# Kernel optimization log

Measured on AMD Instinct MI355X. Metric: run time of the kernel, lower is better.

The kernel has to match this reference:

```python
import jax, jax.numpy as jnp
import numpy as np

D_MODEL = 1024
N_HEAD = 16
D_K = D_MODEL // N_HEAD


def setup_inputs() -> dict:
    key = jax.random.key(0)
    ks = jax.random.split(key, 11)
    B, T = 2, 2048
    s = 1.0 / np.sqrt(D_MODEL)
    return {
        "q": jax.random.normal(ks[0], (B, T, D_MODEL), jnp.float32),
        "k": jax.random.normal(ks[1], (B, T, D_MODEL), jnp.float32),
        "v": jax.random.normal(ks[2], (B, T, D_MODEL), jnp.float32),
        "w_q": jax.random.normal(ks[3], (D_MODEL, D_MODEL), jnp.float32) * s,
        "b_q": jax.random.normal(ks[4], (D_MODEL,), jnp.float32) * 0.01,
        "w_k": jax.random.normal(ks[5], (D_MODEL, D_MODEL), jnp.float32) * s,
        "b_k": jax.random.normal(ks[6], (D_MODEL,), jnp.float32) * 0.01,
        "w_v": jax.random.normal(ks[7], (D_MODEL, D_MODEL), jnp.float32) * s,
        "b_v": jax.random.normal(ks[8], (D_MODEL,), jnp.float32) * 0.01,
        "w_o": jax.random.normal(ks[9], (D_MODEL, D_MODEL), jnp.float32) * s,
        "b_o": jax.random.normal(ks[10], (D_MODEL,), jnp.float32) * 0.01,
    }


def reference(q, k, v, w_q, b_q, w_k, b_k, w_v, b_v, w_o, b_o):
    B, T, _ = q.shape
    # QKV projections -> [B, H, T, d_k]
    def proj(x, w, b):
        return (jnp.einsum('btd,de->bte', x, w) + b).reshape(B, T, N_HEAD, D_K).transpose(0, 2, 1, 3)
    qh = proj(q, w_q, b_q)
    kh = proj(k, w_k, b_k)
    vh = proj(v, w_v, b_v)
    scale = jnp.float32(1.0 / np.sqrt(D_K))
    scores = jnp.einsum('bhqd,bhkd->bhqk', qh, kh) * scale  # [B,H,T,T]
    attn = jax.nn.softmax(scores, axis=-1)
    # dropout is identity in eval mode
    out = jnp.einsum('bhqk,bhkd->bhqd', attn, vh)  # [B,H,T,d_k]
    out = out.transpose(0, 2, 1, 3).reshape(B, T, N_HEAD * D_K)
    return jnp.einsum('btd,de->bte', out, w_o) + b_o
```

## Files before the change

### kernel.cpp

```cpp
#include <hip/hip_runtime.h>
#include <stdint.h>

#define DEVI static __device__ __forceinline__

typedef float f32x4 __attribute__((ext_vector_type(4)));
typedef float f32x16 __attribute__((ext_vector_type(16)));
typedef short s16x8 __attribute__((ext_vector_type(8)));
typedef unsigned short u16x4 __attribute__((ext_vector_type(4)));
typedef uint32_t u32x2 __attribute__((ext_vector_type(2)));
typedef uint32_t u32x4 __attribute__((ext_vector_type(4)));

DEVI unsigned short f2bf(float f) {
  union { float f; uint32_t u; } v; v.f = f;
  uint32_t u = v.u;
  return (unsigned short)((u + 0x7fffu + ((u >> 16) & 1u)) >> 16);
}

DEVI float bf2f(unsigned short u) {
  union { uint32_t u; float f; } v;
  v.u = ((uint32_t)u) << 16;
  return v.f;
}

DEVI uint32_t cvtpk(float lo, float hi) {
  uint32_t r;
  asm("v_cvt_pk_bf16_f32 %0, %1, %2" : "=v"(r) : "v"(lo), "v"(hi));
  return r;
}

DEVI float fexp2(float x) {
#if __has_builtin(__builtin_amdgcn_exp2f)
  return __builtin_amdgcn_exp2f(x);
#else
  return exp2f(x);
#endif
}

DEVI float max3(float a, float b, float c) {
  float r;
  asm("v_max3_f32 %0, %1, %2, %3" : "=v"(r) : "v"(a), "v"(b), "v"(c));
  return r;
}

DEVI void pl32swap(uint32_t& a, uint32_t& b) {
#if __has_builtin(__builtin_amdgcn_permlane32_swap)
  u32x2 r = __builtin_amdgcn_permlane32_swap(a, b, false, false);
  a = r[0]; b = r[1];
#else
  asm("v_permlane32_swap_b32 %0, %1" : "+v"(a), "+v"(b));
#endif
}

DEVI float swap_half(float x, int hi) {
  uint32_t a = __float_as_uint(x), b = a;
  pl32swap(a, b);
  return hi ? __uint_as_float(a) : __uint_as_float(b);
}

DEVI void g2l16(const void* g, void* l) {
  __builtin_amdgcn_global_load_lds(
      (const __attribute__((address_space(1))) void*)g,
      (__attribute__((address_space(3))) void*)l, 16, 0, 0);
}

DEVI float vmax16(const f32x16& v) {
  float a = max3(v[0], v[1], v[2]);
  float b = max3(v[3], v[4], v[5]);
  float c = max3(v[6], v[7], v[8]);
  float d = max3(v[9], v[10], v[11]);
  float e = max3(v[12], v[13], v[14]);
  float x = max3(a, b, c);
  float y = max3(d, e, v[15]);
  return fmaxf(x, y);
}

__global__ __launch_bounds__(256) void k_prep(
    const float* __restrict__ q, const float* __restrict__ k,
    const float* __restrict__ v, unsigned short* __restrict__ qkv,
    const float* __restrict__ w0, const float* __restrict__ w1,
    const float* __restrict__ w2, const float* __restrict__ w3,
    unsigned short* __restrict__ t0, unsigned short* __restrict__ t1,
    unsigned short* __restrict__ t2, unsigned short* __restrict__ t3) {
  __shared__ float tile[32][33];
  const int bx = blockIdx.x;
  if (bx < 3072) {
    const int y = bx >> 10;
    const float* in = y == 0 ? q : y == 1 ? k : v;
    unsigned short* o = qkv + (size_t)y * 4194304;
    int idx = (bx & 1023) * 256 + threadIdx.x;
    for (int i = idx * 4; i < 4194304; i += 1048576) {
      f32x4 x = *(const f32x4*)(in + i);
      u16x4 r;
      for (int j = 0; j < 4; ++j) r[j] = f2bf(x[j]);
      *(u16x4*)(o + i) = r;
    }
  } else {
    const int wb = bx - 3072;
    const int z = wb >> 10, tb = wb & 1023;
    const float* w = z == 0 ? w0 : z == 1 ? w1 : z == 2 ? w2 : w3;
    unsigned short* wt = z == 0 ? t0 : z == 1 ? t1 : z == 2 ? t2 : t3;
    const int n0 = (tb & 31) * 32, k0 = (tb >> 5) * 32;
    const int tx = threadIdx.x & 31, ty = threadIdx.x >> 5;
    for (int j = 0; j < 4; ++j)
      tile[ty + j * 8][tx] = w[(size_t)(k0 + ty + j * 8) * 1024 + n0 + tx];
    __syncthreads();
    for (int j = 0; j < 4; ++j)
      wt[(size_t)(n0 + ty + j * 8) * 1024 + k0 + tx] = f2bf(tile[tx][ty + j * 8]);
  }
}

__global__ __launch_bounds__(256) void k_gemm_multi(
    const unsigned short* A0, const unsigned short* A1, const unsigned short* A2,
    const unsigned short* B0, const unsigned short* B1, const unsigned short* B2,
    const float* c0, const float* c1, const float* c2,
    void* o0, void* o1, void* o2, int mode0) {
  constexpr int K = 1024;
  const int z = blockIdx.y;
  const unsigned short* A = z == 0 ? A0 : z == 1 ? A1 : A2;
  const unsigned short* Bt = z == 0 ? B0 : z == 1 ? B1 : B2;
  const float* bias = z == 0 ? c0 : z == 1 ? c1 : c2;
  void* outp = z == 0 ? o0 : z == 1 ? o1 : o2;
  const int MODE = mode0 + z;

  __shared__ __align__(16) unsigned short As[128 * 64];
  __shared__ __align__(16) unsigned short Bs[64 * 64];
  const int tid = threadIdx.x;
  const int lane = tid & 63, w = tid >> 6;
  const int g = lane >> 4, c = lane & 15;
  const int wgid = (blockIdx.x & 7) * 64 + (blockIdx.x >> 3);
  const int bm = wgid >> 4, bn = wgid & 15;
  const int m0 = bm * 128, n0 = bn * 64;
  const int wr = w >> 1, wc = w & 1;
  f32x4 acc[4][2] = {};

  for (int kt = 0; kt < 16; ++kt) {
    const int k0 = kt * 64;
    __syncthreads();
#pragma unroll
    for (int it = 0; it < 4; ++it) {
      int e = it * 256 + tid;
      int row = e >> 3, cwp = (e & 7) ^ (row & 7);
      g2l16(A + (size_t)(m0 + row) * K + k0 + cwp * 8,
            (char*)As + (it * 256 + (w << 6)) * 16);
    }
#pragma unroll
    for (int it = 0; it < 2; ++it) {
      int e = it * 256 + tid;
      int row = e >> 3, cwp = (e & 7) ^ (row & 7);
      g2l16(Bt + (size_t)(n0 + row) * K + k0 + cwp * 8,
            (char*)Bs + (it * 256 + (w << 6)) * 16);
    }
    __syncthreads();
    for (int kk = 0; kk < 2; ++kk) {
      s16x8 af[4], bfr[2];
      for (int mi = 0; mi < 4; ++mi) {
        int row = wr * 64 + mi * 16 + c;
        int ch = (kk * 4 + g) ^ (row & 7);
        af[mi] = *(const s16x8*)((const char*)As + row * 128 + ch * 16);
      }
      for (int ni = 0; ni < 2; ++ni) {
        int row = wc * 32 + ni * 16 + c;
        int ch = (kk * 4 + g) ^ (row & 7);
        bfr[ni] = *(const s16x8*)((const char*)Bs + row * 128 + ch * 16);
      }
      for (int mi = 0; mi < 4; ++mi)
        for (int ni = 0; ni < 2; ++ni)
          acc[mi][ni] = __builtin_amdgcn_mfma_f32_16x16x32_bf16(
              af[mi], bfr[ni], acc[mi][ni], 0, 0, 0);
    }
  }

  if (MODE == 0 || MODE == 1) {
    unsigned short* out = (unsigned short*)outp;
    const float scale = (MODE == 0) ? 0.1803368801111204f : 1.0f;
    for (int mi = 0; mi < 4; ++mi)
      for (int ni = 0; ni < 2; ++ni) {
        int row = m0 + wr * 64 + mi * 16 + g * 4;
        int col = n0 + wc * 32 + ni * 16 + c;
        float bb = bias[col];
        for (int r = 0; r < 4; ++r)
          out[(size_t)(row + r) * 1024 + col] = f2bf((acc[mi][ni][r] + bb) * scale);
      }
  } else if (MODE == 2) {
    unsigned short* vt = (unsigned short*)outp;
    const int bq = m0 >> 11, t0 = m0 & 2047;
    for (int mi = 0; mi < 4; ++mi)
      for (int ni = 0; ni < 2; ++ni) {
        int rowb = wr * 64 + mi * 16 + g * 4;
        int coll = wc * 32 + ni * 16 + c;
        float bb = bias[n0 + coll];
        u16x4 pk;
        for (int r = 0; r < 4; ++r) pk[r] = f2bf(acc[mi][ni][r] + bb);
        *(u16x4*)(vt + (size_t)(bq * 1024 + n0 + coll) * 2048 + t0 + rowb) = pk;
      }
  } else {
    float* out = (float*)outp;
    for (int mi = 0; mi < 4; ++mi)
      for (int ni = 0; ni < 2; ++ni) {
        int row = m0 + wr * 64 + mi * 16 + g * 4;
        int col = n0 + wc * 32 + ni * 16 + c;
        float bb = bias[col];
        for (int r = 0; r < 4; ++r)
          out[(size_t)(row + r) * 1024 + col] = acc[mi][ni][r] + bb;
      }
  }
}

__global__ __launch_bounds__(256) void k_attn(const unsigned short* __restrict__ Qp,
                                              const unsigned short* __restrict__ Kp,
                                              const unsigned short* __restrict__ Vt,
                                              unsigned short* __restrict__ Po0,
                                              unsigned short* __restrict__ Po1,
                                              float2* __restrict__ ml) {
  __shared__ __align__(16) unsigned short Ks[2][4096];
  __shared__ __align__(16) unsigned short Vs[2][4096];
  const int tid = threadIdx.x;
  const int lane = tid & 63, w = tid >> 6;
  const int l31 = lane & 31, hi = lane >> 5;
  const int blk = (blockIdx.x & 7) * 128 + (blockIdx.x >> 3);
  const int half = blk & 1, qt = (blk >> 1) & 15, bh = blk >> 5;
  const int b = bh >> 4, h = bh & 15;
  const int m0 = qt * 128 + w * 32;
  const size_t qkBase = (size_t)b * 2048 * 1024 + (size_t)h * 64;
  const size_t vtBase = ((size_t)b * 1024 + h * 64) * 2048;

  const unsigned short* qrow = Qp + qkBase + (size_t)(m0 + l31) * 1024;
  s16x8 bq[4];
#pragma unroll
  for (int s = 0; s < 4; ++s)
    bq[s] = *(const s16x8*)(qrow + s * 16 + hi * 8);

  const int r0 = tid >> 3, c0 = tid & 7;
  const int csw = (c0 ^ (r0 & 7)) * 8;
  const unsigned short* ks0 = Kp + qkBase + (size_t)half * 1048576 +
                              (size_t)r0 * 1024 + csw;
  const unsigned short* vs0 = Vt + vtBase + (size_t)r0 * 2048 + half * 1024 + csw;
  const int ldw = w * 1024;

  auto stage = [&](int buf, int t) {
    const size_t ko = (size_t)t * 65536;
    const int vo = t * 64;
    char* kb = (char*)&Ks[buf][0];
    char* vb = (char*)&Vs[buf][0];
    g2l16(ks0 + ko, kb + ldw);
    g2l16(ks0 + ko + 32 * 1024, kb + 4096 + ldw);
    g2l16(vs0 + vo, vb + ldw);
    g2l16(vs0 + vo + 32 * 2048, vb + 4096 + ldw);
  };

  float m_run = -1e30f;
  f32x16 o0 = {}, o1 = {}, la = {};
  const u32x4 onev = {0x3F803F80u, 0x3F803F80u, 0x3F803F80u, 0x3F803F80u};
  const s16x8 ones = *(const s16x8*)&onev;

  stage(0, 0);
  __syncthreads();

  const int rch = l31 & 7;

#pragma unroll 1
  for (int t = 0; t < 16; ++t) {
    const int cur = t & 1;
    if (t < 15) stage(cur ^ 1, t + 1);
    const char* ks = (const char*)&Ks[cur][0];
    const char* vs = (const char*)&Vs[cur][0];

    f32x16 s0 = {}, s1 = {};
    __builtin_amdgcn_s_setprio(1);
#pragma unroll
    for (int ds = 0; ds < 4; ++ds) {
      int ch = (2 * ds + hi) ^ rch;
      s16x8 a0 = *(const s16x8*)(ks + l31 * 128 + ch * 16);
      s16x8 a1 = *(const s16x8*)(ks + (32 + l31) * 128 + ch * 16);
      s0 = __builtin_amdgcn_mfma_f32_32x32x16_bf16(a0, bq[ds], s0, 0, 0, 0);
      s1 = __builtin_amdgcn_mfma_f32_32x32x16_bf16(a1, bq[ds], s1, 0, 0, 0);
    }
    __builtin_amdgcn_s_setprio(0);

    float tm = fmaxf(vmax16(s0), vmax16(s1));
    tm = fmaxf(tm, swap_half(tm, hi));
    if (!__all(tm - m_run <= 8.0f)) {
      float mt = fmaxf(m_run, tm);
      float al = fexp2(m_run - mt);
      la[0] *= al;
#pragma unroll
      for (int j = 0; j < 16; ++j) { o0[j] *= al; o1[j] *= al; }
      m_run = mt;
    }
#pragma unroll
    for (int j = 0; j < 16; ++j) s0[j] = fexp2(s0[j] - m_run);
#pragma unroll
    for (int j = 0; j < 16; ++j) s1[j] = fexp2(s1[j] - m_run);

    s16x8 pf[4];
    {
      uint32_t w0 = cvtpk(s0[0], s0[1]), w1 = cvtpk(s0[2], s0[3]);
      uint32_t w2 = cvtpk(s0[4], s0[5]), w3 = cvtpk(s0[6], s0[7]);
      uint32_t w4 = cvtpk(s0[8], s0[9]), w5 = cvtpk(s0[10], s0[11]);
      uint32_t w6 = cvtpk(s0[12], s0[13]), w7 = cvtpk(s0[14], s0[15]);
      pl32swap(w0, w2); pl32swap(w1, w3); pl32swap(w4, w6); pl32swap(w5, w7);
      u32x4 f0 = {w0, w1, w2, w3}, f1 = {w4, w5, w6, w7};
      pf[0] = *(s16x8*)&f0;
      pf[1] = *(s16x8*)&f1;
    }
    {
      uint32_t w0 = cvtpk(s1[0], s1[1]), w1 = cvtpk(s1[2], s1[3]);
      uint32_t w2 = cvtpk(s1[4], s1[5]), w3 = cvtpk(s1[6], s1[7]);
      uint32_t w4 = cvtpk(s1[8], s1[9]), w5 = cvtpk(s1[10], s1[11]);
      uint32_t w6 = cvtpk(s1[12], s1[13]), w7 = cvtpk(s1[14], s1[15]);
      pl32swap(w0, w2); pl32swap(w1, w3); pl32swap(w4, w6); pl32swap(w5, w7);
      u32x4 f0 = {w0, w1, w2, w3}, f1 = {w4, w5, w6, w7};
      pf[2] = *(s16x8*)&f0;
      pf[3] = *(s16x8*)&f1;
    }

    __builtin_amdgcn_s_setprio(1);
#pragma unroll
    for (int ksp = 0; ksp < 4; ++ksp) {
      int ch = (2 * ksp + hi) ^ rch;
      s16x8 a0 = *(const s16x8*)(vs + l31 * 128 + ch * 16);
      s16x8 a1 = *(const s16x8*)(vs + (32 + l31) * 128 + ch * 16);
      o0 = __builtin_amdgcn_mfma_f32_32x32x16_bf16(a0, pf[ksp], o0, 0, 0, 0);
      o1 = __builtin_amdgcn_mfma_f32_32x32x16_bf16(a1, pf[ksp], o1, 0, 0, 0);
      la = __builtin_amdgcn_mfma_f32_32x32x16_bf16(ones, pf[ksp], la, 0, 0, 0);
    }
    __builtin_amdgcn_s_setprio(0);

    __syncthreads();
  }

  float lt = la[0];
  float inv = 1.0f / lt;
  unsigned short* Po = half ? Po1 : Po0;
  unsigned short* arow = Po + ((size_t)b * 2048 + m0 + l31) * 1024 + h * 64;
#pragma unroll
  for (int dblk = 0; dblk < 2; ++dblk) {
#pragma unroll
    for (int rq = 0; rq < 4; ++rq) {
      float e0 = (dblk ? o1[rq * 4 + 0] : o0[rq * 4 + 0]) * inv;
      float e1 = (dblk ? o1[rq * 4 + 1] : o0[rq * 4 + 1]) * inv;
      float e2 = (dblk ? o1[rq * 4 + 2] : o0[rq * 4 + 2]) * inv;
      float e3 = (dblk ? o1[rq * 4 + 3] : o0[rq * 4 + 3]) * inv;
      u32x2 pk;
      pk[0] = cvtpk(e0, e1);
      pk[1] = cvtpk(e2, e3);
      *(u32x2*)(arow + dblk * 32 + 8 * rq + 4 * hi) = pk;
    }
  }
  if (hi == 0) {
    int qid = ((b << 4) + h) * 2048 + m0 + l31;
    ml[half * 65536 + qid] = {m_run, lt};
  }
}

__global__ __launch_bounds__(256) void k_comb(const unsigned short* __restrict__ Po0,
                                              const unsigned short* __restrict__ Po1,
                                              const float2* __restrict__ ml,
                                              unsigned short* __restrict__ Att) {
  int idx = blockIdx.x * 256 + threadIdx.x;
  int base = idx * 8;
  int qrow = base >> 10, col = base & 1023;
  int h = col >> 6, b = qrow >> 11, t = qrow & 2047;
  int qid = ((b << 4) + h) * 2048 + t;
  float2 p0 = ml[qid], p1 = ml[65536 + qid];
  float ms = fmaxf(p0.x, p1.x);
  float a0 = fexp2(p0.x - ms) * p0.y, a1 = fexp2(p1.x - ms) * p1.y;
  float inv = 1.0f / (a0 + a1);
  float w0 = a0 * inv, w1 = a1 * inv;
  s16x8 v0 = *(const s16x8*)(Po0 + base);
  s16x8 v1 = *(const s16x8*)(Po1 + base);
  u32x4 pk;
#pragma unroll
  for (int j = 0; j < 4; ++j) {
    float e0 = w0 * bf2f((unsigned short)v0[2 * j]) + w1 * bf2f((unsigned short)v1[2 * j]);
    float e1 = w0 * bf2f((unsigned short)v0[2 * j + 1]) + w1 * bf2f((unsigned short)v1[2 * j + 1]);
    pk[j] = cvtpk(e0, e1);
  }
  *(u32x4*)(Att + base) = pk;
}

extern "C" void kernel_launch(void* const* d_in, const int* in_sizes, int n_in,
                              void* d_out, int out_size, void* d_ws, size_t ws_size,
                              hipStream_t stream) {
  const float* q = (const float*)d_in[0];
  const float* k = (const float*)d_in[1];
  const float* v = (const float*)d_in[2];
  const float* w_q = (const float*)d_in[3];
  const float* b_q = (const float*)d_in[4];
  const float* w_k = (const float*)d_in[5];
  const float* b_k = (const float*)d_in[6];
  const float* w_v = (const float*)d_in[7];
  const float* b_v = (const float*)d_in[8];
  const float* w_o = (const float*)d_in[9];
  const float* b_o = (const float*)d_in[10];

  unsigned short* s = (unsigned short*)d_ws;
  unsigned short* qbf = s;
  unsigned short* kbf = s + 4194304;
  unsigned short* vbf = s + 8388608;
  unsigned short* wqT = s + 12582912;
  unsigned short* wkT = s + 13631488;
  unsigned short* wvT = s + 14680064;
  unsigned short* woT = s + 15728640;
  unsigned short* Qp  = s + 16777216;
  unsigned short* Kp  = s + 20971520;
  unsigned short* Vt  = s + 25165824;
  unsigned short* Po0 = qbf;
  unsigned short* Po1 = kbf;
  unsigned short* Att = vbf;
  float2* ml = (float2*)wqT;

  k_prep<<<7168, 256, 0, stream>>>(q, k, v, qbf, w_q, w_k, w_v, w_o,
                                   wqT, wkT, wvT, woT);

  k_gemm_multi<<<dim3(512, 3), 256, 0, stream>>>(
      qbf, kbf, vbf, wqT, wkT, wvT, b_q, b_k, b_v,
      (void*)Qp, (void*)Kp, (void*)Vt, 0);

  k_attn<<<1024, 256, 0, stream>>>(Qp, Kp, Vt, Po0, Po1, ml);

  k_comb<<<2048, 256, 0, stream>>>(Po0, Po1, ml, Att);

  k_gemm_multi<<<dim3(512, 1), 256, 0, stream>>>(
      Att, Att, Att, woT, woT, woT, b_o, b_o, b_o,
      d_out, d_out, d_out, 3);
}
```

Before: 136.9 us.

## Process two query groups per wave in attention and sum row weights on vector ALU

New measurement: 148.8 us. 8.7% more time.

```diff
diff --git a/kernel.cpp b/kernel.cpp
--- a/kernel.cpp
+++ b/kernel.cpp
@@ -72,6 +72,53 @@
   float x = max3(a, b, c);
   float y = max3(d, e, v[15]);
   return fmaxf(x, y);
+}
+
+DEVI float vsum16(const f32x16& v) {
+  float a = (v[0] + v[1]) + (v[2] + v[3]);
+  float b = (v[4] + v[5]) + (v[6] + v[7]);
+  float c = (v[8] + v[9]) + (v[10] + v[11]);
+  float d = (v[12] + v[13]) + (v[14] + v[15]);
+  return (a + b) + (c + d);
+}
+
+DEVI void sm_group(f32x16& s0, f32x16& s1, float& m_run, float& l_run,
+                   f32x16& o0, f32x16& o1, int hi, s16x8 (&pf)[4]) {
+  float tm = fmaxf(vmax16(s0), vmax16(s1));
+  tm = fmaxf(tm, swap_half(tm, hi));
+  if (!__all(tm - m_run <= 8.0f)) {
+    float mt = fmaxf(m_run, tm);
+    float al = fexp2(m_run - mt);
+    l_run *= al;
+#pragma unroll
+    for (int j = 0; j < 16; ++j) { o0[j] *= al; o1[j] *= al; }
+    m_run = mt;
+  }
+#pragma unroll
+  for (int j = 0; j < 16; ++j) s0[j] = fexp2(s0[j] - m_run);
+#pragma unroll
+  for (int j = 0; j < 16; ++j) s1[j] = fexp2(s1[j] - m_run);
+  l_run += vsum16(s0) + vsum16(s1);
+  {
+    uint32_t w0 = cvtpk(s0[0], s0[1]), w1 = cvtpk(s0[2], s0[3]);
+    uint32_t w2 = cvtpk(s0[4], s0[5]), w3 = cvtpk(s0[6], s0[7]);
+    uint32_t w4 = cvtpk(s0[8], s0[9]), w5 = cvtpk(s0[10], s0[11]);
+    uint32_t w6 = cvtpk(s0[12], s0[13]), w7 = cvtpk(s0[14], s0[15]);
+    pl32swap(w0, w2); pl32swap(w1, w3); pl32swap(w4, w6); pl32swap(w5, w7);
+    u32x4 f0 = {w0, w1, w2, w3}, f1 = {w4, w5, w6, w7};
+    pf[0] = *(s16x8*)&f0;
+    pf[1] = *(s16x8*)&f1;
+  }
+  {
+    uint32_t w0 = cvtpk(s1[0], s1[1]), w1 = cvtpk(s1[2], s1[3]);
+    uint32_t w2 = cvtpk(s1[4], s1[5]), w3 = cvtpk(s1[6], s1[7]);
+    uint32_t w4 = cvtpk(s1[8], s1[9]), w5 = cvtpk(s1[10], s1[11]);
+    uint32_t w6 = cvtpk(s1[12], s1[13]), w7 = cvtpk(s1[14], s1[15]);
+    pl32swap(w0, w2); pl32swap(w1, w3); pl32swap(w4, w6); pl32swap(w5, w7);
+    u32x4 f0 = {w0, w1, w2, w3}, f1 = {w4, w5, w6, w7};
+    pf[2] = *(s16x8*)&f0;
+    pf[3] = *(s16x8*)&f1;
+  }
 }
 
 __global__ __launch_bounds__(256) void k_prep(
@@ -217,18 +264,21 @@
   const int tid = threadIdx.x;
   const int lane = tid & 63, w = tid >> 6;
   const int l31 = lane & 31, hi = lane >> 5;
-  const int blk = (blockIdx.x & 7) * 128 + (blockIdx.x >> 3);
-  const int half = blk & 1, qt = (blk >> 1) & 15, bh = blk >> 5;
+  const int blk = (blockIdx.x & 7) * 64 + (blockIdx.x >> 3);
+  const int half = blk & 1, qt = (blk >> 1) & 7, bh = blk >> 4;
   const int b = bh >> 4, h = bh & 15;
-  const int m0 = qt * 128 + w * 32;
+  const int m0 = qt * 256 + w * 64;
   const size_t qkBase = (size_t)b * 2048 * 1024 + (size_t)h * 64;
   const size_t vtBase = ((size_t)b * 1024 + h * 64) * 2048;
 
-  const unsigned short* qrow = Qp + qkBase + (size_t)(m0 + l31) * 1024;
-  s16x8 bq[4];
-#pragma unroll
-  for (int s = 0; s < 4; ++s)
-    bq[s] = *(const s16x8*)(qrow + s * 16 + hi * 8);
+  s16x8 bq[2][4];
+#pragma unroll
+  for (int gq = 0; gq < 2; ++gq) {
+    const unsigned short* qrow = Qp + qkBase + (size_t)(m0 + gq * 32 + l31) * 1024;
+#pragma unroll
+    for (int s = 0; s < 4; ++s)
+      bq[gq][s] = *(const s16x8*)(qrow + s * 16 + hi * 8);
+  }
 
   const int r0 = tid >> 3, c0 = tid & 7;
   const int csw = (c0 ^ (r0 & 7)) * 8;
@@ -248,10 +298,8 @@
     g2l16(vs0 + vo + 32 * 2048, vb + 4096 + ldw);
   };
 
-  float m_run = -1e30f;
-  f32x16 o0 = {}, o1 = {}, la = {};
-  const u32x4 onev = {0x3F803F80u, 0x3F803F80u, 0x3F803F80u, 0x3F803F80u};
-  const s16x8 ones = *(const s16x8*)&onev;
+  float mA = -1e30f, mB = -1e30f, lA = 0.f, lB = 0.f;
+  f32x16 oA0 = {}, oA1 = {}, oB0 = {}, oB1 = {};
 
   stage(0, 0);
   __syncthreads();
@@ -265,91 +313,75 @@
     const char* ks = (const char*)&Ks[cur][0];
     const char* vs = (const char*)&Vs[cur][0];
 
-    f32x16 s0 = {}, s1 = {};
+    f32x16 sA0 = {}, sA1 = {}, sB0 = {}, sB1 = {};
     __builtin_amdgcn_s_setprio(1);
 #pragma unroll
     for (int ds = 0; ds < 4; ++ds) {
       int ch = (2 * ds + hi) ^ rch;
       s16x8 a0 = *(const s16x8*)(ks + l31 * 128 + ch * 16);
       s16x8 a1 = *(const s16x8*)(ks + (32 + l31) * 128 + ch * 16);
-      s0 = __builtin_amdgcn_mfma_f32_32x32x16_bf16(a0, bq[ds], s0, 0, 0, 0);
-      s1 = __builtin_amdgcn_mfma_f32_32x32x16_bf16(a1, bq[ds], s1, 0, 0, 0);
+      sA0 = __builtin_amdgcn_mfma_f32_32x32x16_bf16(a0, bq[0][ds], sA0, 0, 0, 0);
+      sB0 = __builtin_amdgcn_mfma_f32_32x32x16_bf16(a0, bq[1][ds], sB0, 0, 0, 0);
+      sA1 = __builtin_amdgcn_mfma_f32_32x32x16_bf16(a1, bq[0][ds], sA1, 0, 0, 0);
+      sB1 = __builtin_amdgcn_mfma_f32_32x32x16_bf16(a1, bq[1][ds], sB1, 0, 0, 0);
     }
     __builtin_amdgcn_s_setprio(0);
 
-    float tm = fmaxf(vmax16(s0), vmax16(s1));
-    tm = fmaxf(tm, swap_half(tm, hi));
-    if (!__all(tm - m_run <= 8.0f)) {
-      float mt = fmaxf(m_run, tm);
-      float al = fexp2(m_run - mt);
-      la[0] *= al;
-#pragma unroll
-      for (int j = 0; j < 16; ++j) { o0[j] *= al; o1[j] *= al; }
-      m_run = mt;
-    }
-#pragma unroll
-    for (int j = 0; j < 16; ++j) s0[j] = fexp2(s0[j] - m_run);
-#pragma unroll
-    for (int j = 0; j < 16; ++j) s1[j] = fexp2(s1[j] - m_run);
-
-    s16x8 pf[4];
-    {
-      uint32_t w0 = cvtpk(s0[0], s0[1]), w1 = cvtpk(s0[2], s0[3]);
-      uint32_t w2 = cvtpk(s0[4], s0[5]), w3 = cvtpk(s0[6], s0[7]);
-      uint32_t w4 = cvtpk(s0[8], s0[9]), w5 = cvtpk(s0[10], s0[11]);
-      uint32_t w6 = cvtpk(s0[12], s0[13]), w7 = cvtpk(s0[14], s0[15]);
-      pl32swap(w0, w2); pl32swap(w1, w3); pl32swap(w4, w6); pl32swap(w5, w7);
-      u32x4 f0 = {w0, w1, w2, w3}, f1 = {w4, w5, w6, w7};
-      pf[0] = *(s16x8*)&f0;
-      pf[1] = *(s16x8*)&f1;
-    }
-    {
-      uint32_t w0 = cvtpk(s1[0], s1[1]), w1 = cvtpk(s1[2], s1[3]);
-      uint32_t w2 = cvtpk(s1[4], s1[5]), w3 = cvtpk(s1[6], s1[7]);
-      uint32_t w4 = cvtpk(s1[8], s1[9]), w5 = cvtpk(s1[10], s1[11]);
-      uint32_t w6 = cvtpk(s1[12], s1[13]), w7 = cvtpk(s1[14], s1[15]);
-      pl32swap(w0, w2); pl32swap(w1, w3); pl32swap(w4, w6); pl32swap(w5, w7);
-      u32x4 f0 = {w0, w1, w2, w3}, f1 = {w4, w5, w6, w7};
-      pf[2] = *(s16x8*)&f0;
-      pf[3] = *(s16x8*)&f1;
-    }
+    s16x8 pfA[4], pfB[4];
+    sm_group(sA0, sA1, mA, lA, oA0, oA1, hi, pfA);
+    sm_group(sB0, sB1, mB, lB, oB0, oB1, hi, pfB);
 
     __builtin_amdgcn_s_setprio(1);
 #pragma unroll
     for (int ksp = 0; ksp < 4; ++ksp) {
       int ch = (2 * ksp + hi) ^ rch;
-      s16x8 a0 = *(const s16x8*)(vs + l31 * 128 + ch * 16);
-      s16x8 a1 = *(const s16x8*)(vs + (32 + l31) * 128 + ch * 16);
-      o0 = __builtin_amdgcn_mfma_f32_32x32x16_bf16(a0, pf[ksp], o0, 0, 0, 0);
-      o1 = __builtin_amdgcn_mfma_f32_32x32x16_bf16(a1, pf[ksp], o1, 0, 0, 0);
-      la = __builtin_amdgcn_mfma_f32_32x32x16_bf16(ones, pf[ksp], la, 0, 0, 0);
+      s16x8 v0 = *(const s16x8*)(vs + l31 * 128 + ch * 16);
+      s16x8 v1 = *(const s16x8*)(vs + (32 + l31) * 128 + ch * 16);
+      oA0 = __builtin_amdgcn_mfma_f32_32x32x16_bf16(v0, pfA[ksp], oA0, 0, 0, 0);
+      oB0 = __builtin_amdgcn_mfma_f32_32x32x16_bf16(v0, pfB[ksp], oB0, 0, 0, 0);
+      oA1 = __builtin_amdgcn_mfma_f32_32x32x16_bf16(v1, pfA[ksp], oA1, 0, 0, 0);
+      oB1 = __builtin_amdgcn_mfma_f32_32x32x16_bf16(v1, pfB[ksp], oB1, 0, 0, 0);
     }
     __builtin_amdgcn_s_setprio(0);
 
     __syncthreads();
   }
 
-  float lt = la[0];
-  float inv = 1.0f / lt;
   unsigned short* Po = half ? Po1 : Po0;
-  unsigned short* arow = Po + ((size_t)b * 2048 + m0 + l31) * 1024 + h * 64;
-#pragma unroll
-  for (int dblk = 0; dblk < 2; ++dblk) {
-#pragma unroll
-    for (int rq = 0; rq < 4; ++rq) {
-      float e0 = (dblk ? o1[rq * 4 + 0] : o0[rq * 4 + 0]) * inv;
-      float e1 = (dblk ? o1[rq * 4 + 1] : o0[rq * 4 + 1]) * inv;
-      float e2 = (dblk ? o1[rq * 4 + 2] : o0[rq * 4 + 2]) * inv;
-      float e3 = (dblk ? o1[rq * 4 + 3] : o0[rq * 4 + 3]) * inv;
-      u32x2 pk;
-      pk[0] = cvtpk(e0, e1);
-      pk[1] = cvtpk(e2, e3);
-      *(u32x2*)(arow + dblk * 32 + 8 * rq + 4 * hi) = pk;
-    }
-  }
-  if (hi == 0) {
-    int qid = ((b << 4) + h) * 2048 + m0 + l31;
-    ml[half * 65536 + qid] = {m_run, lt};
+#pragma unroll
+  for (int gq = 0; gq < 2; ++gq) {
+    float lr = gq ? lB : lA;
+    float mr = gq ? mB : mA;
+    float lt = lr + swap_half(lr, hi);
+    float inv = 1.0f / lt;
+    unsigned short* arow =
+        Po + ((size_t)b * 2048 + m0 + gq * 32 + l31) * 1024 + h * 64;
+#pragma unroll
+    for (int dblk = 0; dblk < 2; ++dblk) {
+#pragma unroll
+      for (int rq = 0; rq < 4; ++rq) {
+        float e0, e1, e2, e3;
+        if (gq == 0) {
+          e0 = (dblk ? oA1[rq * 4 + 0] : oA0[rq * 4 + 0]) * inv;
+          e1 = (dblk ? oA1[rq * 4 + 1] : oA0[rq * 4 + 1]) * inv;
+          e2 = (dblk ? oA1[rq * 4 + 2] : oA0[rq * 4 + 2]) * inv;
+          e3 = (dblk ? oA1[rq * 4 + 3] : oA0[rq * 4 + 3]) * inv;
+        } else {
+          e0 = (dblk ? oB1[rq * 4 + 0] : oB0[rq * 4 + 0]) * inv;
+          e1 = (dblk ? oB1[rq * 4 + 1] : oB0[rq * 4 + 1]) * inv;
+          e2 = (dblk ? oB1[rq * 4 + 2] : oB0[rq * 4 + 2]) * inv;
+          e3 = (dblk ? oB1[rq * 4 + 3] : oB0[rq * 4 + 3]) * inv;
+        }
+        u32x2 pk;
+        pk[0] = cvtpk(e0, e1);
+        pk[1] = cvtpk(e2, e3);
+        *(u32x2*)(arow + dblk * 32 + 8 * rq + 4 * hi) = pk;
+      }
+    }
+    if (hi == 0) {
+      int qid = ((b << 4) + h) * 2048 + m0 + gq * 32 + l31;
+      ml[half * 65536 + qid] = {mr, lt};
+    }
   }
 }
 
@@ -417,7 +449,7 @@
       qbf, kbf, vbf, wqT, wkT, wvT, b_q, b_k, b_v,
       (void*)Qp, (void*)Kp, (void*)Vt, 0);
 
-  k_attn<<<1024, 256, 0, stream>>>(Qp, Kp, Vt, Po0, Po1, ml);
+  k_attn<<<512, 256, 0, stream>>>(Qp, Kp, Vt, Po0, Po1, ml);
 
   k_comb<<<2048, 256, 0, stream>>>(Po0, Po1, ml, Att);
 
```
